# Kernel optimization log

Measured on AMD Instinct MI355X. Metric: run time of the kernel, lower is better.

Reference implementation:

```python
import jax, jax.numpy as jnp
import numpy as np

# Forest-Ruth symplectic coefficients
THETA = 1.0 / (2.0 - 2.0 ** (1.0 / 3.0))
C1 = THETA / 2.0
C2 = (1.0 - THETA) / 2.0
C3 = (1.0 - THETA) / 2.0
C4 = THETA / 2.0
D1 = THETA
D2 = 1.0 - 2.0 * THETA
D3 = THETA
DT = 0.01          # self.dt
DT_SCALE = 1.0
PI = np.float32(np.pi)


def _wrap_torus(x):
    # topology_id == 1: wrap coordinates onto the torus [-pi, pi)
    return (x + PI) % (2.0 * PI) - PI


def setup_inputs() -> dict:
    key = jax.random.key(0)
    k0, k1, k2, k3, k4 = jax.random.split(key, 5)
    B, D, K = 32768, 512, 64
    x = jax.random.normal(k0, (B, D), jnp.float32)
    v = jax.random.normal(k1, (B, D), jnp.float32)
    force = 0.1 * jax.random.normal(k2, (B, D), jnp.float32)
    U = 0.05 * jax.random.normal(k3, (D, K), jnp.float32)  # low-rank Christoffel factor
    W = 0.05 * jax.random.normal(k4, (K, D), jnp.float32)
    return {"x": x, "v": v, "force": force, "U": U, "W": W, "steps": 4}


def reference(x, v, force, U, W, steps):
    dt = DT * DT_SCALE

    def acceleration(tx, tv):
        # Christoffel contraction Gamma^i_{jk} v^j v^k with low-rank Gamma = U (.)^2 W
        h = tv @ U                 # [B, K]
        christ = (h * h) @ W       # [B, D]
        return -christ + force     # a = -Gamma(v,v) + external force

    cx, cv = x, v
    for _ in range(steps):
        x1 = _wrap_torus(cx + C1 * dt * cv)
        v1 = cv + D1 * dt * acceleration(x1, cv)
        x2 = _wrap_torus(x1 + C2 * dt * v1)
        v2 = v1 + D2 * dt * acceleration(x2, v1)
        x3 = _wrap_torus(x2 + C3 * dt * v2)
        v3 = v2 + D3 * dt * acceleration(x3, v2)
        cx, cv = _wrap_torus(x3 + C4 * dt * v3), v3
    return (cx, cv)
```

## Files before the change

### kernel.cpp

```cpp
#include <hip/hip_runtime.h>


#define NTH 512

#define VF0 0
#define VF1 8192
#define GF0 16384
#define GF1 17408
#define HB  18432
#define FB  20608
#define LDS_WORDS 37120
#define LDS_BYTES (LDS_WORDS*4)

typedef __attribute__((ext_vector_type(8))) short short8;
typedef __attribute__((ext_vector_type(16))) float float16;

__device__ __forceinline__ float wrap_torus(float y) {
    const float PI_F  = 3.14159265358979323846f;
    const float TPI_F = 6.28318530717958647692f;
    float t = y + PI_F;
    if (t >= TPI_F) t -= TPI_F;
    else if (t < 0.0f) t += TPI_F;
    return t - PI_F;
}

__device__ __forceinline__ void split2(float v, unsigned short& hi, unsigned short& lo) {
    unsigned u = __float_as_uint(v);
    unsigned h = (u + 0x7fffu + ((u >> 16) & 1u)) >> 16;
    hi = (unsigned short)h;
    float hf = __uint_as_float(h << 16);
    float r = v - hf;
    unsigned u2 = __float_as_uint(r);
    unsigned l = (u2 + 0x7fffu + ((u2 >> 16) & 1u)) >> 16;
    lo = (unsigned short)l;
}

__device__ __forceinline__ unsigned pack_split(float v) {
    unsigned short hi, lo;
    split2(v, hi, lo);
    return (((unsigned)hi) << 16) | (unsigned)lo;
}

__device__ __forceinline__ void unpack_frag(uint4 l4, uint4 h4, short8& fhi, short8& flo) {
    fhi[0]=(short)(l4.x>>16); flo[0]=(short)(l4.x&0xffffu);
    fhi[1]=(short)(l4.y>>16); flo[1]=(short)(l4.y&0xffffu);
    fhi[2]=(short)(l4.z>>16); flo[2]=(short)(l4.z&0xffffu);
    fhi[3]=(short)(l4.w>>16); flo[3]=(short)(l4.w&0xffffu);
    fhi[4]=(short)(h4.x>>16); flo[4]=(short)(h4.x&0xffffu);
    fhi[5]=(short)(h4.y>>16); flo[5]=(short)(h4.y&0xffffu);
    fhi[6]=(short)(h4.z>>16); flo[6]=(short)(h4.z&0xffffu);
    fhi[7]=(short)(h4.w>>16); flo[7]=(short)(h4.w&0xffffu);
}

__device__ __forceinline__ int swz(int s, int kst) {
    return s ^ ((s >> 5) << 1) ^ (kst & 3);
}

__device__ __forceinline__ void vf_store(unsigned int* ldsu, int m, int d, unsigned p) {
    int kst = d >> 4, lb = (d >> 3) & 1, j = d & 7;
    int slot = swz(m + 32 * lb, kst);
    ldsu[((j >> 2) ? VF1 : VF0) + (kst * 64 + slot) * 4 + (j & 3)] = p;
}

__global__ void fr_prep(const float* __restrict__ Um, const float* __restrict__ Wm,
                        unsigned short* __restrict__ usw, unsigned short* __restrict__ wsw) {
    int tid = blockIdx.x * 256 + threadIdx.x;
    int lane = tid & 63;
    if (tid < 4096) {
        int c   = (tid >> 6) & 7;
        int ks4 = (tid >> 9) & 3;
        int nt1 = (tid >> 11) & 1;
        int fbase = (((nt1 * 4 + ks4) * 8 + c) * 2) * 512;
        #pragma unroll
        for (int j = 0; j < 8; ++j) {
            int d = 128 * ks4 + 16 * c + 8 * (lane >> 5) + j;
            int n = 32 * nt1 + (lane & 31);
            unsigned short hi, lo;
            split2(Um[d * 64 + n], hi, lo);
            usw[fbase + lane * 8 + j] = hi;
            usw[fbase + 512 + lane * 8 + j] = lo;
        }
    } else {
        int id = tid - 4096;
        lane = id & 63;
        int kk = (id >> 6) & 3;
        int nt = (id >> 8) & 15;
        int fbase = ((nt * 4 + kk) * 2) * 512;
        #pragma unroll
        for (int j = 0; j < 8; ++j) {
            int k = 16 * kk + 8 * (lane >> 5) + j;
            int n = 32 * nt + (lane & 31);
            unsigned short hi, lo;
            split2(Wm[k * 512 + n], hi, lo);
            wsw[fbase + lane * 8 + j] = hi;
            wsw[fbase + 512 + lane * 8 + j] = lo;
        }
    }
}

__global__ __launch_bounds__(NTH, 2) void fr_mfma(
    const float* __restrict__ xin, const float* __restrict__ vin,
    const float* __restrict__ fin,
    const short8* __restrict__ usw, const short8* __restrict__ wsw,
    float* __restrict__ xout, float* __restrict__ vout)
{
    extern __shared__ float lds[];
    unsigned int* ldsu = (unsigned int*)lds;

    const int t = threadIdx.x;
    const int lane = t & 63;
    const int w = __builtin_amdgcn_readfirstlane(t >> 6);
    const int nt1 = w & 1;
    const int ks4 = w >> 1;
    const int rhalf = lane >> 5;
    const int R0 = (int)blockIdx.x * 32;

    const double theta = 1.0 / (2.0 - 1.2599210498948732);
    const float c1dt = (float)(theta * 0.5 * 0.01);
    const float c2dt = (float)((1.0 - theta) * 0.5 * 0.01);
    const float d1dt = (float)(theta * 0.01);
    const float d2dt = (float)((1.0 - 2.0 * theta) * 0.01);

    short8 frag[16];
    uintptr_t uop = (uintptr_t)usw;
    uintptr_t wop = (uintptr_t)wsw;
    const int ub = (nt1 * 4 + ks4) * 16;
    const int wb = w * 16;
    {
        const short8* up = (const short8*)uop;
        #pragma unroll
        for (int i = 0; i < 16; ++i)
            frag[i] = up[(ub + i) * 64 + lane];
    }

    float vst[2][16], xst[2][16];
    int cg[2];
    cg[0] = (w * 2 + 0) * 32 + (lane & 31);
    cg[1] = (w * 2 + 1) * 32 + (lane & 31);
    #pragma unroll
    for (int nt = 0; nt < 2; ++nt) {
        #pragma unroll
        for (int r = 0; r < 16; ++r) {
            int rrow = (r & 3) + 8 * (r >> 2) + 4 * rhalf;
            size_t idx = (size_t)(R0 + rrow) * 512 + cg[nt];
            vst[nt][r] = vin[idx];
            xst[nt][r] = xin[idx];
        }
    }

    {
        #pragma unroll
        for (int it = 0; it < 8; ++it) {
            int flat = it * 2048 + t * 4;
            float4 val = *(const float4*)(fin + (size_t)R0 * 512 + flat);
            int row = flat >> 9, col = flat & 511;
            *(float4*)(lds + FB + row * 516 + col) = val;
        }
    }

    #pragma unroll
    for (int nt = 0; nt < 2; ++nt)
        #pragma unroll
        for (int r = 0; r < 16; ++r)
            xst[nt][r] = wrap_torus(xst[nt][r] + c1dt * vst[nt][r]);

    #pragma unroll
    for (int nt = 0; nt < 2; ++nt) {
        #pragma unroll
        for (int r = 0; r < 16; ++r) {
            int m = (r & 3) + 8 * (r >> 2) + 4 * rhalf;
            vf_store(ldsu, m, cg[nt], pack_split(vst[nt][r]));
        }
    }
    for (int i = t; i < 32 * 68; i += NTH) lds[HB + i] = 0.0f;

    #pragma unroll 1
    for (int sub = 0; sub < 12; ++sub) {
        const int idx3 = sub - (sub / 3) * 3;
        const float ddt = (idx3 == 1) ? d2dt : d1dt;
        const float xc  = (idx3 == 2) ? c1dt : c2dt;
        const bool dbl  = (idx3 == 2) && (sub != 11);

        __syncthreads();

        float16 acc0, acc1;
        #pragma unroll
        for (int i = 0; i < 16; ++i) { acc0[i] = 0.0f; acc1[i] = 0.0f; }
        #pragma unroll
        for (int c = 0; c < 8; ++c) {
            int kst = ks4 * 8 + c;
            int slot = swz(lane, kst);
            uint4 pl = *(const uint4*)&ldsu[VF0 + (kst * 64 + slot) * 4];
            uint4 ph = *(const uint4*)&ldsu[VF1 + (kst * 64 + slot) * 4];
            short8 Ahi, Alo;
            unpack_frag(pl, ph, Ahi, Alo);
            acc0 = __builtin_amdgcn_mfma_f32_32x32x16_bf16(Ahi, frag[2 * c],     acc0, 0, 0, 0);
            acc1 = __builtin_amdgcn_mfma_f32_32x32x16_bf16(Alo, frag[2 * c],     acc1, 0, 0, 0);
            acc1 = __builtin_amdgcn_mfma_f32_32x32x16_bf16(Ahi, frag[2 * c + 1], acc1, 0, 0, 0);
        }

        asm volatile("" : "+s"(wop));
        {
            const short8* wp = (const short8*)wop;
            #pragma unroll
            for (int i = 0; i < 16; ++i)
                frag[i] = wp[(wb + i) * 64 + lane];
        }

        {
            int kcol = nt1 * 32 + (lane & 31);
            #pragma unroll
            for (int r = 0; r < 16; ++r) {
                int m = (r & 3) + 8 * (r >> 2) + 4 * rhalf;
                atomicAdd(&lds[HB + m * 68 + kcol], acc0[r] + acc1[r]);
            }
        }
        __syncthreads();

        {
            int grow = t >> 4;
            int k4 = (t & 15) * 4;
            float4 h4 = *(const float4*)&lds[HB + grow * 68 + k4];
            float4 z4; z4.x = 0.0f; z4.y = 0.0f; z4.z = 0.0f; z4.w = 0.0f;
            *(float4*)&lds[HB + grow * 68 + k4] = z4;
            uint4 gp;
            gp.x = pack_split(h4.x * h4.x);
            gp.y = pack_split(h4.y * h4.y);
            gp.z = pack_split(h4.z * h4.z);
            gp.w = pack_split(h4.w * h4.w);
            int kst2 = k4 >> 4, lb2 = (k4 >> 3) & 1, jb = k4 & 7;
            int slot2 = swz(grow + 32 * lb2, kst2);
            *(uint4*)&ldsu[((jb >> 2) ? GF1 : GF0) + (kst2 * 64 + slot2) * 4] = gp;
        }
        __syncthreads();

        float16 cA, cB;
        #pragma unroll
        for (int i = 0; i < 16; ++i) { cA[i] = 0.0f; cB[i] = 0.0f; }
        #pragma unroll
        for (int kk = 0; kk < 4; ++kk) {
            int slot = swz(lane, kk);
            uint4 pl = *(const uint4*)&ldsu[GF0 + (kk * 64 + slot) * 4];
            uint4 ph = *(const uint4*)&ldsu[GF1 + (kk * 64 + slot) * 4];
            short8 Ahi, Alo;
            unpack_frag(pl, ph, Ahi, Alo);
            cA = __builtin_amdgcn_mfma_f32_32x32x16_bf16(Ahi, frag[2 * kk],         cA, 0, 0, 0);
            cB = __builtin_amdgcn_mfma_f32_32x32x16_bf16(Ahi, frag[8 + 2 * kk],     cB, 0, 0, 0);
            cA = __builtin_amdgcn_mfma_f32_32x32x16_bf16(Alo, frag[2 * kk],         cA, 0, 0, 0);
            cB = __builtin_amdgcn_mfma_f32_32x32x16_bf16(Alo, frag[8 + 2 * kk],     cB, 0, 0, 0);
            cA = __builtin_amdgcn_mfma_f32_32x32x16_bf16(Ahi, frag[2 * kk + 1],     cA, 0, 0, 0);
            cB = __builtin_amdgcn_mfma_f32_32x32x16_bf16(Ahi, frag[8 + 2 * kk + 1], cB, 0, 0, 0);
        }

        if (sub != 11) {
            asm volatile("" : "+s"(uop));
            const short8* up = (const short8*)uop;
            #pragma unroll
            for (int i = 0; i < 16; ++i)
                frag[i] = up[(ub + i) * 64 + lane];
        }

        #pragma unroll
        for (int nt = 0; nt < 2; ++nt) {
            #pragma unroll
            for (int r = 0; r < 16; ++r) {
                int m = (r & 3) + 8 * (r >> 2) + 4 * rhalf;
                float fv = lds[FB + m * 516 + cg[nt]];
                float christ = (nt == 0) ? cA[r] : cB[r];
                float vn = vst[nt][r] + ddt * (fv - christ);
                vst[nt][r] = vn;
                float xn = wrap_torus(xst[nt][r] + xc * vn);
                if (dbl) xn = wrap_torus(xn + c1dt * vn);
                xst[nt][r] = xn;
            }
        }

        if (sub != 11) {
            #pragma unroll
            for (int nt = 0; nt < 2; ++nt) {
                #pragma unroll
                for (int r = 0; r < 16; ++r) {
                    int m = (r & 3) + 8 * (r >> 2) + 4 * rhalf;
                    vf_store(ldsu, m, cg[nt], pack_split(vst[nt][r]));
                }
            }
        }
    }

    #pragma unroll
    for (int nt = 0; nt < 2; ++nt) {
        #pragma unroll
        for (int r = 0; r < 16; ++r) {
            int rrow = (r & 3) + 8 * (r >> 2) + 4 * rhalf;
            size_t idx = (size_t)(R0 + rrow) * 512 + cg[nt];
            xout[idx] = xst[nt][r];
            vout[idx] = vst[nt][r];
        }
    }
}

extern "C" void kernel_launch(void* const* d_in, const int* in_sizes, int n_in,
                              void* d_out, int out_size, void* d_ws, size_t ws_size,
                              hipStream_t stream) {
    const float* x = (const float*)d_in[0];
    const float* v = (const float*)d_in[1];
    const float* f = (const float*)d_in[2];
    const float* U = (const float*)d_in[3];
    const float* W = (const float*)d_in[4];

    float* xout = (float*)d_out;
    float* vout = xout + (size_t)32768 * 512;

    unsigned short* usw = (unsigned short*)d_ws;
    unsigned short* wsw = usw + 65536;

    fr_prep<<<32, 256, 0, stream>>>(U, W, usw, wsw);

    hipFuncSetAttribute(reinterpret_cast<const void*>(fr_mfma),
                        hipFuncAttributeMaxDynamicSharedMemorySize, LDS_BYTES);
    fr_mfma<<<1024, NTH, LDS_BYTES, stream>>>(
        x, v, f, (const short8*)usw, (const short8*)wsw, xout, vout);
}
```

Baseline: 1.264 ms.

## Double block to 1024 threads, halving per-wave columns and K-slice

Raises the block from 8 to 16 waves. Each wave now owns one 32-column tile instead of two, and an 8-way instead of a 4-way K split of the first GEMM. The prep kernel re-swizzles the U fragments to match, and per-thread registers (state arrays, fragments, accumulators) are halved to allow more waves per CU. The cost is more LDS atomic adds per row, more waves contending at each barrier, and a higher occupancy target that relies on LDS limits allowing it.

```diff
diff --git a/kernel.cpp b/kernel.cpp
--- a/kernel.cpp
+++ b/kernel.cpp
@@ -1,7 +1,7 @@
 #include <hip/hip_runtime.h>
 
 
-#define NTH 512
+#define NTH 1024
 
 #define VF0 0
 #define VF1 8192
@@ -67,13 +67,13 @@
     int tid = blockIdx.x * 256 + threadIdx.x;
     int lane = tid & 63;
     if (tid < 4096) {
-        int c   = (tid >> 6) & 7;
-        int ks4 = (tid >> 9) & 3;
+        int c   = (tid >> 6) & 3;
+        int ks8 = (tid >> 8) & 7;
         int nt1 = (tid >> 11) & 1;
-        int fbase = (((nt1 * 4 + ks4) * 8 + c) * 2) * 512;
+        int fbase = (((nt1 * 8 + ks8) * 4 + c) * 2) * 512;
         #pragma unroll
         for (int j = 0; j < 8; ++j) {
-            int d = 128 * ks4 + 16 * c + 8 * (lane >> 5) + j;
+            int d = 64 * ks8 + 16 * c + 8 * (lane >> 5) + j;
             int n = 32 * nt1 + (lane & 31);
             unsigned short hi, lo;
             split2(Um[d * 64 + n], hi, lo);
@@ -84,12 +84,12 @@
         int id = tid - 4096;
         lane = id & 63;
         int kk = (id >> 6) & 3;
-        int nt = (id >> 8) & 15;
-        int fbase = ((nt * 4 + kk) * 2) * 512;
+        int ct = (id >> 8) & 15;
+        int fbase = ((ct * 4 + kk) * 2) * 512;
         #pragma unroll
         for (int j = 0; j < 8; ++j) {
             int k = 16 * kk + 8 * (lane >> 5) + j;
-            int n = 32 * nt + (lane & 31);
+            int n = 32 * ct + (lane & 31);
             unsigned short hi, lo;
             split2(Wm[k * 512 + n], hi, lo);
             wsw[fbase + lane * 8 + j] = hi;
@@ -98,7 +98,7 @@
     }
 }
 
-__global__ __launch_bounds__(NTH, 2) void fr_mfma(
+__global__ __launch_bounds__(NTH, 4) void fr_mfma(
     const float* __restrict__ xin, const float* __restrict__ vin,
     const float* __restrict__ fin,
     const short8* __restrict__ usw, const short8* __restrict__ wsw,
@@ -111,9 +111,11 @@
     const int lane = t & 63;
     const int w = __builtin_amdgcn_readfirstlane(t >> 6);
     const int nt1 = w & 1;
-    const int ks4 = w >> 1;
+    const int ks8 = w >> 1;
     const int rhalf = lane >> 5;
     const int R0 = (int)blockIdx.x * 32;
+    const int cg = w * 32 + (lane & 31);
+    const int lslot = lane ^ (rhalf << 1);
 
     const double theta = 1.0 / (2.0 - 1.2599210498948732);
     const float c1dt = (float)(theta * 0.5 * 0.01);
@@ -121,37 +123,31 @@
     const float d1dt = (float)(theta * 0.01);
     const float d2dt = (float)((1.0 - 2.0 * theta) * 0.01);
 
-    short8 frag[16];
+    short8 frag[8];
     uintptr_t uop = (uintptr_t)usw;
     uintptr_t wop = (uintptr_t)wsw;
-    const int ub = (nt1 * 4 + ks4) * 16;
-    const int wb = w * 16;
+    const int ub8 = (nt1 * 8 + ks8) * 8;
+    const int wb8 = w * 8;
     {
         const short8* up = (const short8*)uop;
         #pragma unroll
-        for (int i = 0; i < 16; ++i)
-            frag[i] = up[(ub + i) * 64 + lane];
-    }
-
-    float vst[2][16], xst[2][16];
-    int cg[2];
-    cg[0] = (w * 2 + 0) * 32 + (lane & 31);
-    cg[1] = (w * 2 + 1) * 32 + (lane & 31);
+        for (int i = 0; i < 8; ++i)
+            frag[i] = up[(ub8 + i) * 64 + lane];
+    }
+
+    float vst[16], xst[16];
     #pragma unroll
-    for (int nt = 0; nt < 2; ++nt) {
-        #pragma unroll
-        for (int r = 0; r < 16; ++r) {
-            int rrow = (r & 3) + 8 * (r >> 2) + 4 * rhalf;
-            size_t idx = (size_t)(R0 + rrow) * 512 + cg[nt];
-            vst[nt][r] = vin[idx];
-            xst[nt][r] = xin[idx];
-        }
+    for (int r = 0; r < 16; ++r) {
+        int m = (r & 3) + 8 * (r >> 2) + 4 * rhalf;
+        size_t idx = (size_t)(R0 + m) * 512 + cg;
+        vst[r] = vin[idx];
+        xst[r] = xin[idx];
     }
 
     {
         #pragma unroll
-        for (int it = 0; it < 8; ++it) {
-            int flat = it * 2048 + t * 4;
+        for (int it = 0; it < 4; ++it) {
+            int flat = it * 4096 + t * 4;
             float4 val = *(const float4*)(fin + (size_t)R0 * 512 + flat);
             int row = flat >> 9, col = flat & 511;
             *(float4*)(lds + FB + row * 516 + col) = val;
@@ -159,18 +155,10 @@
     }
 
     #pragma unroll
-    for (int nt = 0; nt < 2; ++nt)
-        #pragma unroll
-        for (int r = 0; r < 16; ++r)
-            xst[nt][r] = wrap_torus(xst[nt][r] + c1dt * vst[nt][r]);
-
-    #pragma unroll
-    for (int nt = 0; nt < 2; ++nt) {
-        #pragma unroll
-        for (int r = 0; r < 16; ++r) {
-            int m = (r & 3) + 8 * (r >> 2) + 4 * rhalf;
-            vf_store(ldsu, m, cg[nt], pack_split(vst[nt][r]));
-        }
+    for (int r = 0; r < 16; ++r) {
+        xst[r] = wrap_torus(xst[r] + c1dt * vst[r]);
+        int m = (r & 3) + 8 * (r >> 2) + 4 * rhalf;
+        vf_store(ldsu, m, cg, pack_split(vst[r]));
     }
     for (int i = t; i < 32 * 68; i += NTH) lds[HB + i] = 0.0f;
 
@@ -183,28 +171,28 @@
 
         __syncthreads();
 
-        float16 acc0, acc1;
-        #pragma unroll
-        for (int i = 0; i < 16; ++i) { acc0[i] = 0.0f; acc1[i] = 0.0f; }
-        #pragma unroll
-        for (int c = 0; c < 8; ++c) {
-            int kst = ks4 * 8 + c;
-            int slot = swz(lane, kst);
+        float16 acc;
+        #pragma unroll
+        for (int i = 0; i < 16; ++i) acc[i] = 0.0f;
+        #pragma unroll
+        for (int c = 0; c < 4; ++c) {
+            int kst = ks8 * 4 + c;
+            int slot = lslot ^ (kst & 3);
             uint4 pl = *(const uint4*)&ldsu[VF0 + (kst * 64 + slot) * 4];
             uint4 ph = *(const uint4*)&ldsu[VF1 + (kst * 64 + slot) * 4];
             short8 Ahi, Alo;
             unpack_frag(pl, ph, Ahi, Alo);
-            acc0 = __builtin_amdgcn_mfma_f32_32x32x16_bf16(Ahi, frag[2 * c],     acc0, 0, 0, 0);
-            acc1 = __builtin_amdgcn_mfma_f32_32x32x16_bf16(Alo, frag[2 * c],     acc1, 0, 0, 0);
-            acc1 = __builtin_amdgcn_mfma_f32_32x32x16_bf16(Ahi, frag[2 * c + 1], acc1, 0, 0, 0);
+            acc = __builtin_amdgcn_mfma_f32_32x32x16_bf16(Ahi, frag[2 * c],     acc, 0, 0, 0);
+            acc = __builtin_amdgcn_mfma_f32_32x32x16_bf16(Alo, frag[2 * c],     acc, 0, 0, 0);
+            acc = __builtin_amdgcn_mfma_f32_32x32x16_bf16(Ahi, frag[2 * c + 1], acc, 0, 0, 0);
         }
 
         asm volatile("" : "+s"(wop));
         {
             const short8* wp = (const short8*)wop;
             #pragma unroll
-            for (int i = 0; i < 16; ++i)
-                frag[i] = wp[(wb + i) * 64 + lane];
+            for (int i = 0; i < 8; ++i)
+                frag[i] = wp[(wb8 + i) * 64 + lane];
         }
 
         {
@@ -212,90 +200,67 @@
             #pragma unroll
             for (int r = 0; r < 16; ++r) {
                 int m = (r & 3) + 8 * (r >> 2) + 4 * rhalf;
-                atomicAdd(&lds[HB + m * 68 + kcol], acc0[r] + acc1[r]);
+                atomicAdd(&lds[HB + m * 68 + kcol], acc[r]);
             }
         }
         __syncthreads();
 
         {
-            int grow = t >> 4;
-            int k4 = (t & 15) * 4;
-            float4 h4 = *(const float4*)&lds[HB + grow * 68 + k4];
-            float4 z4; z4.x = 0.0f; z4.y = 0.0f; z4.z = 0.0f; z4.w = 0.0f;
-            *(float4*)&lds[HB + grow * 68 + k4] = z4;
-            uint4 gp;
-            gp.x = pack_split(h4.x * h4.x);
-            gp.y = pack_split(h4.y * h4.y);
-            gp.z = pack_split(h4.z * h4.z);
-            gp.w = pack_split(h4.w * h4.w);
-            int kst2 = k4 >> 4, lb2 = (k4 >> 3) & 1, jb = k4 & 7;
+            int grow = t >> 5;
+            int k2 = (t & 31) * 2;
+            float2 h2 = *(const float2*)&lds[HB + grow * 68 + k2];
+            float2 z2; z2.x = 0.0f; z2.y = 0.0f;
+            *(float2*)&lds[HB + grow * 68 + k2] = z2;
+            uint2 gp;
+            gp.x = pack_split(h2.x * h2.x);
+            gp.y = pack_split(h2.y * h2.y);
+            int kst2 = k2 >> 4, lb2 = (k2 >> 3) & 1, jb = k2 & 7;
             int slot2 = swz(grow + 32 * lb2, kst2);
-            *(uint4*)&ldsu[((jb >> 2) ? GF1 : GF0) + (kst2 * 64 + slot2) * 4] = gp;
+            *(uint2*)&ldsu[((jb >> 2) ? GF1 : GF0) + (kst2 * 64 + slot2) * 4 + (jb & 3)] = gp;
         }
         __syncthreads();
 
-        float16 cA, cB;
-        #pragma unroll
-        for (int i = 0; i < 16; ++i) { cA[i] = 0.0f; cB[i] = 0.0f; }
+        #pragma unroll
+        for (int i = 0; i < 16; ++i) acc[i] = 0.0f;
         #pragma unroll
         for (int kk = 0; kk < 4; ++kk) {
-            int slot = swz(lane, kk);
+            int slot = lslot ^ kk;
             uint4 pl = *(const uint4*)&ldsu[GF0 + (kk * 64 + slot) * 4];
             uint4 ph = *(const uint4*)&ldsu[GF1 + (kk * 64 + slot) * 4];
             short8 Ahi, Alo;
             unpack_frag(pl, ph, Ahi, Alo);
-            cA = __builtin_amdgcn_mfma_f32_32x32x16_bf16(Ahi, frag[2 * kk],         cA, 0, 0, 0);
-            cB = __builtin_amdgcn_mfma_f32_32x32x16_bf16(Ahi, frag[8 + 2 * kk],     cB, 0, 0, 0);
-            cA = __builtin_amdgcn_mfma_f32_32x32x16_bf16(Alo, frag[2 * kk],         cA, 0, 0, 0);
-            cB = __builtin_amdgcn_mfma_f32_32x32x16_bf16(Alo, frag[8 + 2 * kk],     cB, 0, 0, 0);
-            cA = __builtin_amdgcn_mfma_f32_32x32x16_bf16(Ahi, frag[2 * kk + 1],     cA, 0, 0, 0);
-            cB = __builtin_amdgcn_mfma_f32_32x32x16_bf16(Ahi, frag[8 + 2 * kk + 1], cB, 0, 0, 0);
+            acc = __builtin_amdgcn_mfma_f32_32x32x16_bf16(Ahi, frag[2 * kk],     acc, 0, 0, 0);
+            acc = __builtin_amdgcn_mfma_f32_32x32x16_bf16(Alo, frag[2 * kk],     acc, 0, 0, 0);
+            acc = __builtin_amdgcn_mfma_f32_32x32x16_bf16(Ahi, frag[2 * kk + 1], acc, 0, 0, 0);
         }
 
         if (sub != 11) {
             asm volatile("" : "+s"(uop));
             const short8* up = (const short8*)uop;
             #pragma unroll
-            for (int i = 0; i < 16; ++i)
-                frag[i] = up[(ub + i) * 64 + lane];
-        }
-
-        #pragma unroll
-        for (int nt = 0; nt < 2; ++nt) {
-            #pragma unroll
-            for (int r = 0; r < 16; ++r) {
-                int m = (r & 3) + 8 * (r >> 2) + 4 * rhalf;
-                float fv = lds[FB + m * 516 + cg[nt]];
-                float christ = (nt == 0) ? cA[r] : cB[r];
-                float vn = vst[nt][r] + ddt * (fv - christ);
-                vst[nt][r] = vn;
-                float xn = wrap_torus(xst[nt][r] + xc * vn);
-                if (dbl) xn = wrap_torus(xn + c1dt * vn);
-                xst[nt][r] = xn;
-            }
-        }
-
-        if (sub != 11) {
-            #pragma unroll
-            for (int nt = 0; nt < 2; ++nt) {
-                #pragma unroll
-                for (int r = 0; r < 16; ++r) {
-                    int m = (r & 3) + 8 * (r >> 2) + 4 * rhalf;
-                    vf_store(ldsu, m, cg[nt], pack_split(vst[nt][r]));
-                }
-            }
+            for (int i = 0; i < 8; ++i)
+                frag[i] = up[(ub8 + i) * 64 + lane];
+        }
+
+        #pragma unroll
+        for (int r = 0; r < 16; ++r) {
+            int m = (r & 3) + 8 * (r >> 2) + 4 * rhalf;
+            float fv = lds[FB + m * 516 + cg];
+            float vn = vst[r] + ddt * (fv - acc[r]);
+            vst[r] = vn;
+            float xn = wrap_torus(xst[r] + xc * vn);
+            if (dbl) xn = wrap_torus(xn + c1dt * vn);
+            xst[r] = xn;
+            if (sub != 11) vf_store(ldsu, m, cg, pack_split(vn));
         }
     }
 
     #pragma unroll
-    for (int nt = 0; nt < 2; ++nt) {
-        #pragma unroll
-        for (int r = 0; r < 16; ++r) {
-            int rrow = (r & 3) + 8 * (r >> 2) + 4 * rhalf;
-            size_t idx = (size_t)(R0 + rrow) * 512 + cg[nt];
-            xout[idx] = xst[nt][r];
-            vout[idx] = vst[nt][r];
-        }
+    for (int r = 0; r < 16; ++r) {
+        int m = (r & 3) + 8 * (r >> 2) + 4 * rhalf;
+        size_t idx = (size_t)(R0 + m) * 512 + cg;
+        xout[idx] = xst[r];
+        vout[idx] = vst[r];
     }
 }
 
```

Result: slower. 1.838 ms (+45.4%).

## Fuse h-squared split into GEMM2 fragment loads and double-buffer H accumulator

Applied to the files above, without the earlier changes.

Removes the intermediate pass that squared, bf16-split and repacked the H accumulator into a swizzled G buffer, along with one block-wide barrier per substep. Each wave now reads raw H floats from LDS and squares and splits them directly into MFMA fragments. H is double-buffered so the next buffer can be zeroed without an extra barrier. The cost is redundant split work across waves and non-swizzled LDS reads that may hit bank conflicts.

```diff
diff --git a/kernel.cpp b/kernel.cpp
--- a/kernel.cpp
+++ b/kernel.cpp
@@ -5,11 +5,10 @@
 
 #define VF0 0
 #define VF1 8192
-#define GF0 16384
-#define GF1 17408
-#define HB  18432
-#define FB  20608
-#define LDS_WORDS 37120
+#define HB0W 16384
+#define HBSZ 2176
+#define FB  20736
+#define LDS_WORDS 37248
 #define LDS_BYTES (LDS_WORDS*4)
 
 typedef __attribute__((ext_vector_type(8))) short short8;
@@ -52,6 +51,13 @@
     fhi[7]=(short)(h4.w>>16); flo[7]=(short)(h4.w&0xffffu);
 }
 
+__device__ __forceinline__ void gsplit(float h, short8& fhi, short8& flo, int j) {
+    unsigned short hi, lo;
+    split2(h * h, hi, lo);
+    fhi[j] = (short)hi;
+    flo[j] = (short)lo;
+}
+
 __device__ __forceinline__ int swz(int s, int kst) {
     return s ^ ((s >> 5) << 1) ^ (kst & 3);
 }
@@ -113,6 +119,7 @@
     const int nt1 = w & 1;
     const int ks4 = w >> 1;
     const int rhalf = lane >> 5;
+    const int hrow = lane & 31;
     const int R0 = (int)blockIdx.x * 32;
 
     const double theta = 1.0 / (2.0 - 1.2599210498948732);
@@ -172,7 +179,7 @@
             vf_store(ldsu, m, cg[nt], pack_split(vst[nt][r]));
         }
     }
-    for (int i = t; i < 32 * 68; i += NTH) lds[HB + i] = 0.0f;
+    for (int i = t; i < 2 * HBSZ; i += NTH) lds[HB0W + i] = 0.0f;
 
     #pragma unroll 1
     for (int sub = 0; sub < 12; ++sub) {
@@ -180,6 +187,8 @@
         const float ddt = (idx3 == 1) ? d2dt : d1dt;
         const float xc  = (idx3 == 2) ? c1dt : c2dt;
         const bool dbl  = (idx3 == 2) && (sub != 11);
+        const int hbc = HB0W + (sub & 1) * HBSZ;
+        const int hbn = HB0W + ((sub + 1) & 1) * HBSZ;
 
         __syncthreads();
 
@@ -212,44 +221,38 @@
             #pragma unroll
             for (int r = 0; r < 16; ++r) {
                 int m = (r & 3) + 8 * (r >> 2) + 4 * rhalf;
-                atomicAdd(&lds[HB + m * 68 + kcol], acc0[r] + acc1[r]);
+                atomicAdd(&lds[hbc + m * 68 + kcol], acc0[r] + acc1[r]);
             }
         }
         __syncthreads();
 
-        {
-            int grow = t >> 4;
-            int k4 = (t & 15) * 4;
-            float4 h4 = *(const float4*)&lds[HB + grow * 68 + k4];
-            float4 z4; z4.x = 0.0f; z4.y = 0.0f; z4.z = 0.0f; z4.w = 0.0f;
-            *(float4*)&lds[HB + grow * 68 + k4] = z4;
-            uint4 gp;
-            gp.x = pack_split(h4.x * h4.x);
-            gp.y = pack_split(h4.y * h4.y);
-            gp.z = pack_split(h4.z * h4.z);
-            gp.w = pack_split(h4.w * h4.w);
-            int kst2 = k4 >> 4, lb2 = (k4 >> 3) & 1, jb = k4 & 7;
-            int slot2 = swz(grow + 32 * lb2, kst2);
-            *(uint4*)&ldsu[((jb >> 2) ? GF1 : GF0) + (kst2 * 64 + slot2) * 4] = gp;
-        }
-        __syncthreads();
-
         float16 cA, cB;
         #pragma unroll
         for (int i = 0; i < 16; ++i) { cA[i] = 0.0f; cB[i] = 0.0f; }
         #pragma unroll
         for (int kk = 0; kk < 4; ++kk) {
-            int slot = swz(lane, kk);
-            uint4 pl = *(const uint4*)&ldsu[GF0 + (kk * 64 + slot) * 4];
-            uint4 ph = *(const uint4*)&ldsu[GF1 + (kk * 64 + slot) * 4];
+            int ha = hbc + hrow * 68 + 16 * kk + 8 * rhalf;
+            float4 hA = *(const float4*)&lds[ha];
+            float4 hB = *(const float4*)&lds[ha + 4];
             short8 Ahi, Alo;
-            unpack_frag(pl, ph, Ahi, Alo);
+            gsplit(hA.x, Ahi, Alo, 0);
+            gsplit(hA.y, Ahi, Alo, 1);
+            gsplit(hA.z, Ahi, Alo, 2);
+            gsplit(hA.w, Ahi, Alo, 3);
+            gsplit(hB.x, Ahi, Alo, 4);
+            gsplit(hB.y, Ahi, Alo, 5);
+            gsplit(hB.z, Ahi, Alo, 6);
+            gsplit(hB.w, Ahi, Alo, 7);
             cA = __builtin_amdgcn_mfma_f32_32x32x16_bf16(Ahi, frag[2 * kk],         cA, 0, 0, 0);
             cB = __builtin_amdgcn_mfma_f32_32x32x16_bf16(Ahi, frag[8 + 2 * kk],     cB, 0, 0, 0);
             cA = __builtin_amdgcn_mfma_f32_32x32x16_bf16(Alo, frag[2 * kk],         cA, 0, 0, 0);
             cB = __builtin_amdgcn_mfma_f32_32x32x16_bf16(Alo, frag[8 + 2 * kk],     cB, 0, 0, 0);
             cA = __builtin_amdgcn_mfma_f32_32x32x16_bf16(Ahi, frag[2 * kk + 1],     cA, 0, 0, 0);
             cB = __builtin_amdgcn_mfma_f32_32x32x16_bf16(Ahi, frag[8 + 2 * kk + 1], cB, 0, 0, 0);
+        }
+
+        if (sub != 11) {
+            for (int i = t; i < HBSZ; i += NTH) lds[hbn + i] = 0.0f;
         }
 
         if (sub != 11) {
```

Result: faster. 1.224 ms (-3.1%).
